# Optimization experiments

Hardware: AMD Instinct MI355X
Metric: run time of the kernel (lower is better)

Reference implementation:

```python
import jax, jax.numpy as jnp
import numpy as np

SEQ, B, D_IN, D_H = 1024, 64, 256, 256


def setup_inputs() -> dict:
    key = jax.random.key(0)
    ks = jax.random.split(key, 9)
    scale = 1.0 / np.sqrt(D_IN + D_H)
    inputs = jax.random.normal(ks[0], (SEQ, B, D_IN), dtype=jnp.float32)
    def lin(k):
        kw, kb = jax.random.split(k)
        W = jax.random.uniform(kw, (D_IN + D_H, D_H), jnp.float32, -scale, scale)
        b = jax.random.uniform(kb, (D_H,), jnp.float32, -scale, scale)
        return W, b
    Wf, bf = lin(ks[1])
    Wi, bi = lin(ks[2])
    Wg, bg = lin(ks[3])
    Wo, bo = lin(ks[4])
    return {"inputs": inputs, "Wf": Wf, "bf": bf, "Wi": Wi, "bi": bi,
            "Wg": Wg, "bg": bg, "Wo": Wo, "bo": bo}


def reference(inputs, Wf, bf, Wi, bi, Wg, bg, Wo, bo):
    B_ = inputs.shape[1]
    hx0 = jnp.zeros((B_, D_H), dtype=inputs.dtype)
    cx0 = jnp.zeros((B_, D_H), dtype=inputs.dtype)

    def step(carry, x):
        hx, cx = carry
        comb = jnp.concatenate([x, hx], axis=1)  # [B, D_IN + D_H]
        f = jax.nn.sigmoid(comb @ Wf + bf)
        i = jax.nn.sigmoid(comb @ Wi + bi)
        g = jnp.tanh(comb @ Wg + bg)
        o = jax.nn.sigmoid(comb @ Wo + bo)
        cx = f * cx + i * g
        hx = o * jnp.tanh(cx)
        return (hx, cx), hx

    (hx, cx), outputs = jax.lax.scan(step, (hx0, cx0), inputs)
    return outputs, hx, cx
```

## Files before the change

kernel.cpp:

```cpp
#include <hip/hip_runtime.h>
#include <hip/hip_bf16.h>


typedef _Float16 f16;
typedef _Float16 f16x4 __attribute__((ext_vector_type(4)));
typedef _Float16 f16x8 __attribute__((ext_vector_type(8)));
typedef float f32x4 __attribute__((ext_vector_type(4)));
typedef int i32x4 __attribute__((ext_vector_type(4)));

#define SEQ 1024
#define BATCH 64
#define DIN 256
#define DH 256
#define NCOL 1024

#define WXP_OFF   0u
#define WHQ_OFF   524288u
#define SCL_OFF   786432u
#define BIAS_OFF  790528u
#define HXS8_OFF  794624u
#define CXS_OFF   811008u
#define XP_OFF    876544u

__device__ __forceinline__ float fast_sigmoid(float x) {
  float e = __expf(-x);
  return __builtin_amdgcn_rcpf(1.0f + e);
}
__device__ __forceinline__ float fast_tanh(float x) {
  x = fminf(fmaxf(x, -15.0f), 15.0f);
  float e = __expf(2.0f * x);
  return (e - 1.0f) * __builtin_amdgcn_rcpf(e + 1.0f);
}
__device__ __forceinline__ void lds_barrier() {
  asm volatile("s_waitcnt lgkmcnt(0)\n\ts_barrier" ::: "memory");
}
__device__ __forceinline__ i32x4 MQ(i32x4 a, i32x4 b, i32x4 c) {
  return __builtin_amdgcn_mfma_i32_16x16x64_i8(a, b, c, 0, 0, 0);
}

__global__ void qlstm_prep(const float* __restrict__ Wf, const float* __restrict__ Wi,
                           const float* __restrict__ Wg, const float* __restrict__ Wo,
                           const float* __restrict__ bf_, const float* __restrict__ bi_,
                           const float* __restrict__ bg_, const float* __restrict__ bo_,
                           f16* __restrict__ Wxp, float* __restrict__ biasp) {
  int tid = blockIdx.x * 256 + threadIdx.x;
  if (tid < 4 * 256 * 256) {
    int g = tid >> 16;
    int rem = tid & 65535;
    int k = rem >> 8, n = rem & 255;
    const float* W = (g == 0) ? Wf : (g == 1) ? Wi : (g == 2) ? Wg : Wo;
    float v = W[k * 256 + n];
    int j = (g << 8) + n;
    Wxp[((size_t)(k >> 3) * 1024 + j) * 8 + (k & 7)] = (f16)v;
  }
  if (tid < 1024) {
    int g = tid >> 8, n = tid & 255;
    const float* bb = (g == 0) ? bf_ : (g == 1) ? bi_ : (g == 2) ? bg_ : bo_;
    biasp[tid] = bb[n];
  }
}

__global__ __launch_bounds__(256) void qlstm_prepq(
    const float* __restrict__ Wf, const float* __restrict__ Wi,
    const float* __restrict__ Wg, const float* __restrict__ Wo,
    char* __restrict__ WhQ, float* __restrict__ scl) {
  int j = blockIdx.x * 256 + threadIdx.x;
  if (j >= 1024) return;
  int g = j >> 8, n = j & 255;
  const float* W = (g == 0) ? Wf : (g == 1) ? Wi : (g == 2) ? Wg : Wo;
  float mx = 0.0f;
  for (int r = 0; r < 256; ++r) mx = fmaxf(mx, fabsf(W[(256 + r) * 256 + n]));
  float s = (mx > 0.0f) ? mx * (1.0f / 127.0f) : 1.0f;
  float inv = 1.0f / s;
  int w = n >> 4, c = n & 15;
  size_t tb = (size_t)((w * 4 + g) * 4) * 1024;
  for (int r = 0; r < 256; ++r) {
    float v = W[(256 + r) * 256 + n];
    int q = (int)rintf(v * inv);
    q = q > 127 ? 127 : (q < -127 ? -127 : q);
    int kt = r >> 6, kp = r & 63;
    int lane = (kp >> 4) * 16 + c, jj = kp & 15;
    WhQ[tb + (size_t)kt * 1024 + lane * 16 + jj] = (char)q;
  }
  scl[j] = s * (1.0f / 127.0f);
}

__global__ __launch_bounds__(256) void qlstm_xproj(
    const float* __restrict__ X, const f16* __restrict__ Wxp,
    const float* __restrict__ biasp, f16* __restrict__ Xp2) {
  __shared__ f16 As[128][72];
  __shared__ f16 Bs[8 * 128 * 8];

  int tid = threadIdx.x;
  int tm = blockIdx.x, tn = blockIdx.y;
  int wave = tid >> 6, lane = tid & 63;
  int qm = (wave & 1) * 64, qn = (wave >> 1) * 64;
  int lm = lane & 15, lk = lane >> 4;

  f32x4 acc[4][4];
#pragma unroll
  for (int a = 0; a < 4; ++a)
#pragma unroll
    for (int b = 0; b < 4; ++b) acc[a][b] = (f32x4)0.0f;

  for (int k0 = 0; k0 < 256; k0 += 64) {
    {
      int r = tid >> 1, c0 = (tid & 1) * 32;
      const float4* src = (const float4*)(X + (size_t)(tm * 128 + r) * 256 + k0 + c0);
#pragma unroll
      for (int i = 0; i < 8; ++i) {
        float4 v = src[i];
        f16x4 pk = {(f16)v.x, (f16)v.y, (f16)v.z, (f16)v.w};
        *(f16x4*)&As[r][c0 + i * 4] = pk;
      }
    }
    {
#pragma unroll
      for (int it = 0; it < 4; ++it) {
        int idx = it * 256 + tid;
        int kgi = idx >> 7, n = idx & 127;
        ((uint4*)Bs)[idx] =
            *(const uint4*)(Wxp + (((size_t)(k0 >> 3) + kgi) * 1024 + tn * 128 + n) * 8);
      }
    }
    __syncthreads();
#pragma unroll
    for (int ks = 0; ks < 2; ++ks) {
      f16x8 af[4], bfr[4];
#pragma unroll
      for (int mi = 0; mi < 4; ++mi)
        af[mi] = *(const f16x8*)&As[qm + mi * 16 + lm][ks * 32 + lk * 8];
#pragma unroll
      for (int ni = 0; ni < 4; ++ni)
        bfr[ni] = *(const f16x8*)&Bs[(((ks * 4 + lk) * 128) + qn + ni * 16 + lm) * 8];
#pragma unroll
      for (int mi = 0; mi < 4; ++mi)
#pragma unroll
        for (int ni = 0; ni < 4; ++ni)
          acc[mi][ni] = __builtin_amdgcn_mfma_f32_16x16x32_f16(af[mi], bfr[ni],
                                                               acc[mi][ni], 0, 0, 0);
    }
    __syncthreads();
  }
  int m0 = tm * 128 + qm, j0 = tn * 128 + qn;
#pragma unroll
  for (int mi = 0; mi < 4; ++mi)
#pragma unroll
    for (int ni = 0; ni < 4; ++ni) {
      int j = j0 + ni * 16 + lm;
      int gg = j >> 8, hh = j & 255;
      float bv = biasp[j];
#pragma unroll
      for (int r = 0; r < 4; ++r) {
        int m = m0 + mi * 16 + lk * 4 + r;
        Xp2[((size_t)m * 256 + hh) * 4 + gg] = (f16)(acc[mi][ni][r] + bv);
      }
    }
}

__global__ __launch_bounds__(1024, 4) void qlstm_seq(
    const f16* __restrict__ Xp2, const i32x4* __restrict__ WhQ,
    const float* __restrict__ scl,
    float* __restrict__ out, char* __restrict__ hxs8, float* __restrict__ cxs,
    float* __restrict__ hxout, float* __restrict__ cxout, int t0, int t1) {
  __shared__ char hxq[2][256];

  int tid = threadIdx.x;
  int wv = tid >> 6, lane = tid & 63, c = lane & 15;
  int b = blockIdx.x;
  int h = wv * 16 + c;

  i32x4 wq[4][4];
  {
    const i32x4* wp = WhQ + (size_t)(wv * 16) * 64 + lane;
#pragma unroll
    for (int g = 0; g < 4; ++g)
#pragma unroll
      for (int kt = 0; kt < 4; ++kt) wq[g][kt] = wp[(g * 4 + kt) * 64];
  }
  float sc[4];
#pragma unroll
  for (int g = 0; g < 4; ++g) sc[g] = scl[g * 256 + h];

  int par0 = t0 & 1;
  if (tid < 16) {
    uint4 v;
    if (t0 == 0) v = uint4{0u, 0u, 0u, 0u};
    else v = ((const uint4*)(hxs8 + (size_t)b * 256))[tid];
    *(uint4*)(&hxq[par0][tid * 16]) = v;
  }
  float cx = (t0 != 0) ? cxs[(size_t)b * 256 + h] : 0.0f;

  __syncthreads();

  int koff = (lane >> 4) << 4;
  float hv = 0.0f;
  for (int t = t0; t < t1; ++t) {
    int par = t & 1, parn = par ^ 1;
    const char* hp = &hxq[par][0];

    uint2 xr = *(const uint2*)(Xp2 + (((size_t)(t - t0) * BATCH + b) * 256 + h) * 4);

    i32x4 acc0{}, acc1{}, acc2{}, acc3{};
    i32x4 a0 = *(const i32x4*)(hp + koff);
    i32x4 a1 = *(const i32x4*)(hp + 64 + koff);
    acc0 = MQ(a0, wq[0][0], acc0); acc1 = MQ(a0, wq[1][0], acc1);
    acc2 = MQ(a0, wq[2][0], acc2); acc3 = MQ(a0, wq[3][0], acc3);
    a0 = *(const i32x4*)(hp + 128 + koff);
    acc0 = MQ(a1, wq[0][1], acc0); acc1 = MQ(a1, wq[1][1], acc1);
    acc2 = MQ(a1, wq[2][1], acc2); acc3 = MQ(a1, wq[3][1], acc3);
    a1 = *(const i32x4*)(hp + 192 + koff);
    acc0 = MQ(a0, wq[0][2], acc0); acc1 = MQ(a0, wq[1][2], acc1);
    acc2 = MQ(a0, wq[2][2], acc2); acc3 = MQ(a0, wq[3][2], acc3);
    acc0 = MQ(a1, wq[0][3], acc0); acc1 = MQ(a1, wq[1][3], acc1);
    acc2 = MQ(a1, wq[2][3], acc2); acc3 = MQ(a1, wq[3][3], acc3);

    f16x4 xh = __builtin_bit_cast(f16x4, xr);
    float p0 = fmaf((float)acc0[0], sc[0], (float)xh[0]);
    float p1 = fmaf((float)acc1[0], sc[1], (float)xh[1]);
    float p2 = fmaf((float)acc2[0], sc[2], (float)xh[2]);
    float p3 = fmaf((float)acc3[0], sc[3], (float)xh[3]);

    float vf = fast_sigmoid(p0);
    float vi = fast_sigmoid(p1);
    float vg = fast_tanh(p2);
    float vo = fast_sigmoid(p3);
    cx = fmaf(vf, cx, vi * vg);
    hv = vo * fast_tanh(cx);

    if (lane < 16) {
      out[((size_t)t * BATCH + b) * 256 + h] = hv;
      hxq[parn][h] = (char)(int)rintf(hv * 127.0f);
    }
    lds_barrier();
  }

  if (tid < 16)
    ((uint4*)(hxs8 + (size_t)b * 256))[tid] = *(const uint4*)(&hxq[t1 & 1][tid * 16]);
  if (lane < 16) {
    cxs[(size_t)b * 256 + h] = cx;
    if (t1 == SEQ) {
      hxout[(size_t)b * 256 + h] = hv;
      cxout[(size_t)b * 256 + h] = cx;
    }
  }
}

extern "C" void kernel_launch(void* const* d_in, const int* in_sizes, int n_in,
                              void* d_out, int out_size, void* d_ws, size_t ws_size,
                              hipStream_t stream) {
  const float* X  = (const float*)d_in[0];
  const float* Wf = (const float*)d_in[1]; const float* bf_ = (const float*)d_in[2];
  const float* Wi = (const float*)d_in[3]; const float* bi_ = (const float*)d_in[4];
  const float* Wg = (const float*)d_in[5]; const float* bg_ = (const float*)d_in[6];
  const float* Wo = (const float*)d_in[7]; const float* bo_ = (const float*)d_in[8];
  float* out = (float*)d_out;

  char* ws = (char*)d_ws;
  f16*   Wxp   = (f16*)(ws + WXP_OFF);
  char*  WhQ   = (char*)(ws + WHQ_OFF);
  float* scl   = (float*)(ws + SCL_OFF);
  float* biasp = (float*)(ws + BIAS_OFF);
  char*  hxs8  = (char*)(ws + HXS8_OFF);
  float* cxs   = (float*)(ws + CXS_OFF);
  f16*   Xp2   = (f16*)(ws + XP_OFF);

  size_t avail = (ws_size > XP_OFF) ? (ws_size - XP_OFF) : 0;
  int Tc = SEQ;
  while (Tc > 2 && (size_t)Tc * BATCH * NCOL * 2 > avail) Tc >>= 1;

  qlstm_prep<<<1024, 256, 0, stream>>>(Wf, Wi, Wg, Wo, bf_, bi_, bg_, bo_,
                                       Wxp, biasp);
  qlstm_prepq<<<4, 256, 0, stream>>>(Wf, Wi, Wg, Wo, WhQ, scl);

  float* hxout = out + (size_t)SEQ * BATCH * DH;
  float* cxout = hxout + BATCH * DH;

  for (int t0 = 0; t0 < SEQ; t0 += Tc) {
    dim3 g1(Tc * BATCH / 128, NCOL / 128);
    qlstm_xproj<<<g1, 256, 0, stream>>>(X + (size_t)t0 * BATCH * DIN, Wxp, biasp, Xp2);
    qlstm_seq<<<BATCH, 1024, 0, stream>>>(Xp2, (const i32x4*)WhQ, scl, out, hxs8, cxs,
                                          hxout, cxout, t0, t0 + Tc);
  }
}
```

Baseline: 1.319 ms.

## Parallelize weight quantization prep and interleave gate columns in projection output

The int8 quantization prep previously ran in 4 blocks, each thread looping serially over 256 rows twice. It is now split into an atomicMax column-max kernel and a 1024-block quantize kernel with one element per thread, to cut that serial prep latency. The input projection column order is interleaved (n*4+g), so the output is written contiguously instead of through a gate-strided scatter. Minor changes hoist all hidden-state LDS loads before the MFMAs and move the LDS write ahead of the global store. The extra kernel launch and atomics add small overhead.

```diff
diff --git a/kernel.cpp b/kernel.cpp
--- a/kernel.cpp
+++ b/kernel.cpp
@@ -20,7 +20,8 @@
 #define BIAS_OFF  790528u
 #define HXS8_OFF  794624u
 #define CXS_OFF   811008u
-#define XP_OFF    876544u
+#define SMX_OFF   876544u
+#define XP_OFF    880640u
 
 __device__ __forceinline__ float fast_sigmoid(float x) {
   float e = __expf(-x);
@@ -42,7 +43,8 @@
                            const float* __restrict__ Wg, const float* __restrict__ Wo,
                            const float* __restrict__ bf_, const float* __restrict__ bi_,
                            const float* __restrict__ bg_, const float* __restrict__ bo_,
-                           f16* __restrict__ Wxp, float* __restrict__ biasp) {
+                           f16* __restrict__ Wxp, float* __restrict__ biasp,
+                           int* __restrict__ smx) {
   int tid = blockIdx.x * 256 + threadIdx.x;
   if (tid < 4 * 256 * 256) {
     int g = tid >> 16;
@@ -50,39 +52,49 @@
     int k = rem >> 8, n = rem & 255;
     const float* W = (g == 0) ? Wf : (g == 1) ? Wi : (g == 2) ? Wg : Wo;
     float v = W[k * 256 + n];
-    int j = (g << 8) + n;
+    int j = n * 4 + g;
     Wxp[((size_t)(k >> 3) * 1024 + j) * 8 + (k & 7)] = (f16)v;
   }
   if (tid < 1024) {
     int g = tid >> 8, n = tid & 255;
     const float* bb = (g == 0) ? bf_ : (g == 1) ? bi_ : (g == 2) ? bg_ : bo_;
-    biasp[tid] = bb[n];
-  }
+    biasp[n * 4 + g] = bb[n];
+    smx[tid] = 0;
+  }
+}
+
+__global__ __launch_bounds__(256) void qlstm_prepmax(
+    const float* __restrict__ Wf, const float* __restrict__ Wi,
+    const float* __restrict__ Wg, const float* __restrict__ Wo,
+    int* __restrict__ smx) {
+  int bk = blockIdx.x;
+  int g = bk & 3, r0 = (bk >> 2) * 32;
+  int n = threadIdx.x;
+  const float* W = (g == 0) ? Wf : (g == 1) ? Wi : (g == 2) ? Wg : Wo;
+  float pm = 0.0f;
+  for (int r = 0; r < 32; ++r)
+    pm = fmaxf(pm, fabsf(W[(size_t)(256 + r0 + r) * 256 + n]));
+  atomicMax(&smx[g * 256 + n], __float_as_int(pm));
 }
 
 __global__ __launch_bounds__(256) void qlstm_prepq(
     const float* __restrict__ Wf, const float* __restrict__ Wi,
     const float* __restrict__ Wg, const float* __restrict__ Wo,
-    char* __restrict__ WhQ, float* __restrict__ scl) {
-  int j = blockIdx.x * 256 + threadIdx.x;
-  if (j >= 1024) return;
-  int g = j >> 8, n = j & 255;
+    const int* __restrict__ smx, char* __restrict__ WhQ, float* __restrict__ scl) {
+  int bk = blockIdx.x;
+  int g = bk & 3, r = bk >> 2;
+  int n = threadIdx.x;
   const float* W = (g == 0) ? Wf : (g == 1) ? Wi : (g == 2) ? Wg : Wo;
-  float mx = 0.0f;
-  for (int r = 0; r < 256; ++r) mx = fmaxf(mx, fabsf(W[(256 + r) * 256 + n]));
+  float mx = __int_as_float(smx[g * 256 + n]);
   float s = (mx > 0.0f) ? mx * (1.0f / 127.0f) : 1.0f;
-  float inv = 1.0f / s;
+  float v = W[(size_t)(256 + r) * 256 + n];
+  int q = (int)rintf(v * (1.0f / s));
+  q = q > 127 ? 127 : (q < -127 ? -127 : q);
   int w = n >> 4, c = n & 15;
-  size_t tb = (size_t)((w * 4 + g) * 4) * 1024;
-  for (int r = 0; r < 256; ++r) {
-    float v = W[(256 + r) * 256 + n];
-    int q = (int)rintf(v * inv);
-    q = q > 127 ? 127 : (q < -127 ? -127 : q);
-    int kt = r >> 6, kp = r & 63;
-    int lane = (kp >> 4) * 16 + c, jj = kp & 15;
-    WhQ[tb + (size_t)kt * 1024 + lane * 16 + jj] = (char)q;
-  }
-  scl[j] = s * (1.0f / 127.0f);
+  int kt = r >> 6, kp = r & 63;
+  int lane = (kp >> 4) * 16 + c, jj = kp & 15;
+  WhQ[((size_t)((w * 16 + g * 4 + kt) * 64 + lane)) * 16 + jj] = (char)q;
+  if (r == 0) scl[g * 256 + n] = s * (1.0f / 127.0f);
 }
 
 __global__ __launch_bounds__(256) void qlstm_xproj(
@@ -148,12 +160,11 @@
 #pragma unroll
     for (int ni = 0; ni < 4; ++ni) {
       int j = j0 + ni * 16 + lm;
-      int gg = j >> 8, hh = j & 255;
       float bv = biasp[j];
 #pragma unroll
       for (int r = 0; r < 4; ++r) {
         int m = m0 + mi * 16 + lk * 4 + r;
-        Xp2[((size_t)m * 256 + hh) * 4 + gg] = (f16)(acc[mi][ni][r] + bv);
+        Xp2[(size_t)m * 1024 + j] = (f16)(acc[mi][ni][r] + bv);
       }
     }
 }
@@ -201,19 +212,20 @@
 
     uint2 xr = *(const uint2*)(Xp2 + (((size_t)(t - t0) * BATCH + b) * 256 + h) * 4);
 
-    i32x4 acc0{}, acc1{}, acc2{}, acc3{};
     i32x4 a0 = *(const i32x4*)(hp + koff);
     i32x4 a1 = *(const i32x4*)(hp + 64 + koff);
+    i32x4 a2 = *(const i32x4*)(hp + 128 + koff);
+    i32x4 a3 = *(const i32x4*)(hp + 192 + koff);
+
+    i32x4 acc0{}, acc1{}, acc2{}, acc3{};
     acc0 = MQ(a0, wq[0][0], acc0); acc1 = MQ(a0, wq[1][0], acc1);
     acc2 = MQ(a0, wq[2][0], acc2); acc3 = MQ(a0, wq[3][0], acc3);
-    a0 = *(const i32x4*)(hp + 128 + koff);
     acc0 = MQ(a1, wq[0][1], acc0); acc1 = MQ(a1, wq[1][1], acc1);
     acc2 = MQ(a1, wq[2][1], acc2); acc3 = MQ(a1, wq[3][1], acc3);
-    a1 = *(const i32x4*)(hp + 192 + koff);
-    acc0 = MQ(a0, wq[0][2], acc0); acc1 = MQ(a0, wq[1][2], acc1);
-    acc2 = MQ(a0, wq[2][2], acc2); acc3 = MQ(a0, wq[3][2], acc3);
-    acc0 = MQ(a1, wq[0][3], acc0); acc1 = MQ(a1, wq[1][3], acc1);
-    acc2 = MQ(a1, wq[2][3], acc2); acc3 = MQ(a1, wq[3][3], acc3);
+    acc0 = MQ(a2, wq[0][2], acc0); acc1 = MQ(a2, wq[1][2], acc1);
+    acc2 = MQ(a2, wq[2][2], acc2); acc3 = MQ(a2, wq[3][2], acc3);
+    acc0 = MQ(a3, wq[0][3], acc0); acc1 = MQ(a3, wq[1][3], acc1);
+    acc2 = MQ(a3, wq[2][3], acc2); acc3 = MQ(a3, wq[3][3], acc3);
 
     f16x4 xh = __builtin_bit_cast(f16x4, xr);
     float p0 = fmaf((float)acc0[0], sc[0], (float)xh[0]);
@@ -229,8 +241,8 @@
     hv = vo * fast_tanh(cx);
 
     if (lane < 16) {
+      hxq[parn][h] = (char)(int)rintf(hv * 127.0f);
       out[((size_t)t * BATCH + b) * 256 + h] = hv;
-      hxq[parn][h] = (char)(int)rintf(hv * 127.0f);
     }
     lds_barrier();
   }
@@ -263,6 +275,7 @@
   float* biasp = (float*)(ws + BIAS_OFF);
   char*  hxs8  = (char*)(ws + HXS8_OFF);
   float* cxs   = (float*)(ws + CXS_OFF);
+  int*   smx   = (int*)(ws + SMX_OFF);
   f16*   Xp2   = (f16*)(ws + XP_OFF);
 
   size_t avail = (ws_size > XP_OFF) ? (ws_size - XP_OFF) : 0;
@@ -270,8 +283,9 @@
   while (Tc > 2 && (size_t)Tc * BATCH * NCOL * 2 > avail) Tc >>= 1;
 
   qlstm_prep<<<1024, 256, 0, stream>>>(Wf, Wi, Wg, Wo, bf_, bi_, bg_, bo_,
-                                       Wxp, biasp);
-  qlstm_prepq<<<4, 256, 0, stream>>>(Wf, Wi, Wg, Wo, WhQ, scl);
+                                       Wxp, biasp, smx);
+  qlstm_prepmax<<<32, 256, 0, stream>>>(Wf, Wi, Wg, Wo, smx);
+  qlstm_prepq<<<1024, 256, 0, stream>>>(Wf, Wi, Wg, Wo, smx, WhQ, scl);
 
   float* hxout = out + (size_t)SEQ * BATCH * DH;
   float* cxout = hxout + BATCH * DH;
```

Measured after the change: 1.161 ms. 1.14x faster.
